# Optimization experiments

Measured on AMD Instinct MI355X. Metric: run time of the kernel, lower is better.

The kernel has to match this reference:

```python
import jax, jax.numpy as jnp
import numpy as np

D_MODEL = 768
D_STATE = 16
D_CONV = 4
EXPAND = 2
INNER = EXPAND * D_MODEL  # 1536
BATCH = 2
SEQLEN = 2048


def setup_inputs() -> dict:
    key = jax.random.key(0)
    ks = jax.random.split(key, 8)
    s = 0.02
    return {
        "hidden_states": jax.random.normal(ks[0], (BATCH, SEQLEN, D_MODEL), jnp.float32),
        "in_proj_w": jax.random.normal(ks[1], (2 * INNER, D_MODEL), jnp.float32) * (D_MODEL ** -0.5),
        "out_proj_w": jax.random.normal(ks[2], (D_MODEL, INNER), jnp.float32) * (INNER ** -0.5),
        "dt_proj_w": jax.random.normal(ks[3], (INNER, INNER), jnp.float32) * (INNER ** -0.5),
        "dt_proj_b": jnp.zeros((INNER,), jnp.float32),
        "conv_w": jax.random.normal(ks[4], (INNER, D_CONV), jnp.float32) * s,
        "conv_b": jnp.zeros((INNER,), jnp.float32),
        "A_log": jnp.zeros((INNER, D_STATE), jnp.float32),
        "B_param": jax.random.normal(ks[5], (INNER, D_STATE), jnp.float32) * s,
        "C_param": jax.random.normal(ks[6], (INNER, D_STATE), jnp.float32) * s,
        "D_param": jnp.ones((INNER,), jnp.float32),
        "dt_bias": jnp.zeros((INNER,), jnp.float32),
    }


def reference(hidden_states, in_proj_w, out_proj_w, dt_proj_w, dt_proj_b,
              conv_w, conv_b, A_log, B_param, C_param, D_param, dt_bias):
    # in_proj: (B, L, d_model) -> (B, L, 2*inner); split into projected / gate
    xz = jnp.einsum('bld,od->blo', hidden_states, in_proj_w)
    proj, gate = jnp.split(xz, 2, axis=-1)
    x = jnp.transpose(proj, (0, 2, 1))  # (B, inner, L) channel-first

    # depthwise causal conv (left-pad d_conv-1) + bias + SiLU
    conv = jax.lax.conv_general_dilated(
        x, conv_w[:, None, :], window_strides=(1,),
        padding=[(D_CONV - 1, 0)], feature_group_count=INNER,
        dimension_numbers=('NCH', 'OIH', 'NCH'))
    u = jax.nn.silu(conv + conv_b[None, :, None])  # (B, inner, L)

    # dt projection (1x1 linear on channel-first) + softplus(dt + dt_bias)
    delta = jnp.einsum('oc,bcl->bol', dt_proj_w, u) + dt_proj_b[None, :, None]
    dt = jax.nn.softplus(delta + dt_bias[None, :, None])  # (B, inner, L)

    A = -jnp.exp(A_log)  # (inner, d_state)
    # discretize: dA = exp(dt * A), dBu = dt * u * B   -> (B, inner, L, N)
    dA = jnp.exp(dt[..., None] * A[None, :, None, :])
    dBu = (dt * u)[..., None] * B_param[None, :, None, :]

    dA_t = jnp.moveaxis(dA, 2, 0)    # (L, B, inner, N)
    dBu_t = jnp.moveaxis(dBu, 2, 0)  # (L, B, inner, N)

    def step(h, inp):
        a_t, b_t = inp
        h = a_t * h + b_t                      # (B, inner, N)
        y = jnp.einsum('bdn,dn->bd', h, C_param)
        return h, y

    h0 = jnp.zeros(dA_t.shape[1:], dA.dtype)
    _, ys = jax.lax.scan(step, h0, (dA_t, dBu_t))  # ys: (L, B, inner)
    y = jnp.transpose(ys, (1, 2, 0))               # (B, inner, L)

    z = jnp.transpose(gate, (0, 2, 1))             # (B, inner, L)
    y = (y + D_param[None, :, None] * u) * jax.nn.silu(z)

    # out_proj: (B, inner, L) -> (B, L, d_model)
    return jnp.einsum('bdl,od->blo', y, out_proj_w)
```

## Files before the change

kernel.cpp:

```cpp
#include <hip/hip_runtime.h>
#include <cstdint>
#include <cstddef>

#define D_MODEL 768
#define D_STATE 16
#define D_CONV  4
#define INNER   1536
#define BATCH   2
#define SEQLEN  2048
#define M_TOK   (BATCH * SEQLEN)
#define NCH     (BATCH * INNER)
#define NCHUNK  64
#define CL      (SEQLEN / NCHUNK)

typedef unsigned short u16;
typedef __attribute__((ext_vector_type(4))) unsigned short us4;
typedef __attribute__((ext_vector_type(8))) short bf8;
typedef __attribute__((ext_vector_type(4))) float f32x4;

__device__ __forceinline__ u16 f2bf(float f) {
    uint32_t x = __float_as_uint(f);
    return (u16)((x + 0x7fffu + ((x >> 16) & 1u)) >> 16);
}
__device__ __forceinline__ float bf2f(u16 h) {
    return __uint_as_float(((uint32_t)h) << 16);
}

__global__ __launch_bounds__(256) void cvt_hilo4(
    const float* __restrict__ s0, u16* __restrict__ h0, u16* __restrict__ l0, int n0,
    const float* __restrict__ s1, u16* __restrict__ h1, u16* __restrict__ l1, int n1,
    const float* __restrict__ s2, u16* __restrict__ h2, u16* __restrict__ l2, int n2,
    const float* __restrict__ s3, u16* __restrict__ h3, u16* __restrict__ l3, int n3)
{
    int j = blockIdx.x * 256 + threadIdx.x;
    const float* s; u16* hh; u16* ll;
    if (j < n0) { s = s0; hh = h0; ll = l0; }
    else {
        j -= n0;
        if (j < n1) { s = s1; hh = h1; ll = l1; }
        else {
            j -= n1;
            if (j < n2) { s = s2; hh = h2; ll = l2; }
            else {
                j -= n2;
                if (j >= n3) return;
                s = s3; hh = h3; ll = l3;
            }
        }
    }
    const float4 v = ((const float4*)s)[j];
    us4 h, l;
    h.x = f2bf(v.x); l.x = f2bf(v.x - bf2f(h.x));
    h.y = f2bf(v.y); l.y = f2bf(v.y - bf2f(h.y));
    h.z = f2bf(v.z); l.z = f2bf(v.z - bf2f(h.z));
    h.w = f2bf(v.w); l.w = f2bf(v.w - bf2f(h.w));
    ((us4*)hh)[j] = h;
    ((us4*)ll)[j] = l;
}

template <int MODE, int FRM, int FRN>
__global__ __launch_bounds__(256) void gemm_mfma(
    const u16* __restrict__ Ah_g, const u16* __restrict__ Al_g,
    const u16* __restrict__ Bh_g, const u16* __restrict__ Bl_g,
    float* __restrict__ C, const float* __restrict__ bias1,
    const float* __restrict__ bias2, int M, int N, int K)
{
    constexpr int BM = FRM * 32;
    constexpr int BN = FRN * 32;
    constexpr int SBUF = (BM + BN) * 128;
    __shared__ __align__(16) char smem[2 * SBUF];

    const int tid = threadIdx.x;
    const int w = tid >> 6;
    const int lane = tid & 63;

    const int gx = gridDim.x;
    const int nwg = gx * gridDim.y;
    int f = blockIdx.y * gx + blockIdx.x;
    f = (f & 7) * (nwg >> 3) + (f >> 3);
    const int bm = (f / gx) * BM;
    const int bn = (f % gx) * BN;

    const int wm = (w >> 1) * (FRM * 16);
    const int wn = (w & 1) * (FRN * 16);

    const int g8 = lane & 7;
    const int r8 = lane >> 3;
    const int srcg = g8 ^ r8;
    const int scol = (srcg & 3) * 8;
    const bool use_lo = (srcg & 4) != 0;

    const u16* pA[FRM];
    const u16* pB[FRN];
#pragma unroll
    for (int c = 0; c < FRM; ++c) {
        const int row = w * (FRM * 8) + c * 8 + r8;
        pA[c] = (use_lo ? Al_g : Ah_g) + (size_t)(bm + row) * K + scol;
    }
#pragma unroll
    for (int c = 0; c < FRN; ++c) {
        const int row = w * (FRN * 8) + c * 8 + r8;
        pB[c] = (use_lo ? Bl_g : Bh_g) + (size_t)(bn + row) * K + scol;
    }

    f32x4 acc[FRM][FRN] = {};
    const int fr = lane & 15;
    const int gk = lane >> 4;
    const int ghi = gk ^ (fr & 7);

    const int aoff_h = (wm + fr) * 128 + ghi * 16;
    const int aoff_l = (wm + fr) * 128 + (ghi ^ 4) * 16;
    const int boff_h = BM * 128 + (wn + fr) * 128 + ghi * 16;
    const int boff_l = BM * 128 + (wn + fr) * 128 + (ghi ^ 4) * 16;
    const char* const S0 = smem;
    const char* const S1 = smem + SBUF;

    const int nt = K >> 5;

#define STAGE_ALL(sb, kt)                                                           \
    {                                                                               \
        _Pragma("unroll")                                                           \
        for (int c = 0; c < FRM; ++c)                                               \
            __builtin_amdgcn_global_load_lds(                                       \
                (const __attribute__((address_space(1))) void*)(pA[c] + (kt)),      \
                (__attribute__((address_space(3))) void*)((char*)(sb) + (w * FRM + c) * 1024), \
                16, 0, 0);                                                          \
        _Pragma("unroll")                                                           \
        for (int c = 0; c < FRN; ++c)                                               \
            __builtin_amdgcn_global_load_lds(                                       \
                (const __attribute__((address_space(1))) void*)(pB[c] + (kt)),      \
                (__attribute__((address_space(3))) void*)((char*)(sb) + BM * 128 + (w * FRN + c) * 1024), \
                16, 0, 0);                                                          \
    }

#define WAIT_COUNTED()                                                              \
    if constexpr (FRM + FRN == 8) { asm volatile("s_waitcnt vmcnt(8)" ::: "memory"); } \
    else if constexpr (FRM + FRN == 6) { asm volatile("s_waitcnt vmcnt(6)" ::: "memory"); } \
    else { asm volatile("s_waitcnt vmcnt(4)" ::: "memory"); }

#define COMPUTE(S)                                                                  \
    {                                                                               \
        bf8 ah[FRM], al[FRM], bh[FRN], bl[FRN];                                     \
        _Pragma("unroll")                                                           \
        for (int i = 0; i < FRM; ++i) {                                             \
            ah[i] = *(const bf8*)((S) + aoff_h + i * 2048);                         \
            al[i] = *(const bf8*)((S) + aoff_l + i * 2048);                         \
        }                                                                           \
        _Pragma("unroll")                                                           \
        for (int j = 0; j < FRN; ++j) {                                             \
            bh[j] = *(const bf8*)((S) + boff_h + j * 2048);                         \
            bl[j] = *(const bf8*)((S) + boff_l + j * 2048);                         \
        }                                                                           \
        _Pragma("unroll")                                                           \
        for (int i = 0; i < FRM; ++i)                                               \
            _Pragma("unroll")                                                       \
            for (int j = 0; j < FRN; ++j) {                                         \
                acc[i][j] = __builtin_amdgcn_mfma_f32_16x16x32_bf16(ah[i], bh[j], acc[i][j], 0, 0, 0); \
                acc[i][j] = __builtin_amdgcn_mfma_f32_16x16x32_bf16(ah[i], bl[j], acc[i][j], 0, 0, 0); \
                acc[i][j] = __builtin_amdgcn_mfma_f32_16x16x32_bf16(al[i], bh[j], acc[i][j], 0, 0, 0); \
            }                                                                       \
    }

    STAGE_ALL(S0, 0)

    for (int t = 0; t < nt; t += 2) {
        STAGE_ALL(S1, (t + 1) * 32)
        WAIT_COUNTED()
        __builtin_amdgcn_s_barrier();
        __builtin_amdgcn_sched_barrier(0);
        __builtin_amdgcn_s_setprio(1);
        COMPUTE(S0)
        __builtin_amdgcn_s_setprio(0);
        __builtin_amdgcn_sched_barrier(0);
        __builtin_amdgcn_s_barrier();

        const int k2 = (t + 2 < nt) ? (t + 2) * 32 : (nt - 1) * 32;
        STAGE_ALL(S0, k2)
        WAIT_COUNTED()
        __builtin_amdgcn_s_barrier();
        __builtin_amdgcn_sched_barrier(0);
        __builtin_amdgcn_s_setprio(1);
        COMPUTE(S1)
        __builtin_amdgcn_s_setprio(0);
        __builtin_amdgcn_sched_barrier(0);
        __builtin_amdgcn_s_barrier();
    }
#undef STAGE_ALL
#undef WAIT_COUNTED
#undef COMPUTE

    const int r0 = (lane >> 4) * 4;
#pragma unroll
    for (int i = 0; i < FRM; ++i) {
        const int row0 = bm + wm + i * 16 + r0;
#pragma unroll
        for (int j = 0; j < FRN; ++j) {
            const int col = bn + wn + j * 16 + fr;
            float add = 0.f;
            if constexpr (MODE == 1) add = bias1[col] + bias2[col];
#pragma unroll
            for (int r = 0; r < 4; ++r) {
                float v = acc[i][j][r];
                if constexpr (MODE == 1) {
                    const float xx = v + add;
                    v = (xx > 20.f) ? xx : log1pf(expf(xx));
                }
                C[(size_t)(row0 + r) * N + col] = v;
            }
        }
    }
}

__global__ __launch_bounds__(256) void conv_silu_kernel(
    const float* __restrict__ xz, const float* __restrict__ cw,
    const float* __restrict__ cb, u16* __restrict__ uh, u16* __restrict__ ul)
{
    const int idx = blockIdx.x * 256 + threadIdx.x;
    const int c4 = (idx % (INNER / 4)) * 4;
    const int m  = idx / (INNER / 4);
    if (m >= M_TOK) return;
    const int b = m >> 11;
    const int l = m & (SEQLEN - 1);

    float wt[4][4];
#pragma unroll
    for (int i = 0; i < 4; ++i) {
        const float4 wv = *(const float4*)&cw[(c4 + i) * 4];
        wt[i][0] = wv.x; wt[i][1] = wv.y; wt[i][2] = wv.z; wt[i][3] = wv.w;
    }
    const float4 bias = *(const float4*)&cb[c4];
    float a[4] = {bias.x, bias.y, bias.z, bias.w};

#pragma unroll
    for (int j = 0; j < 4; ++j) {
        const int ll = l - 3 + j;
        if (ll >= 0) {
            const float4 x = *(const float4*)&xz[(size_t)(b * SEQLEN + ll) * (2 * INNER) + c4];
            a[0] = fmaf(x.x, wt[0][j], a[0]);
            a[1] = fmaf(x.y, wt[1][j], a[1]);
            a[2] = fmaf(x.z, wt[2][j], a[2]);
            a[3] = fmaf(x.w, wt[3][j], a[3]);
        }
    }
    float o[4];
#pragma unroll
    for (int i = 0; i < 4; ++i) o[i] = a[i] / (1.f + __expf(-a[i]));

    us4 h, lo;
    h.x = f2bf(o[0]); lo.x = f2bf(o[0] - bf2f(h.x));
    h.y = f2bf(o[1]); lo.y = f2bf(o[1] - bf2f(h.y));
    h.z = f2bf(o[2]); lo.z = f2bf(o[2] - bf2f(h.z));
    h.w = f2bf(o[3]); lo.w = f2bf(o[3] - bf2f(h.w));
    const size_t vi = ((size_t)m * INNER + c4) / 4;
    ((us4*)uh)[vi] = h;
    ((us4*)ul)[vi] = lo;
}

__global__ __launch_bounds__(256) void scan_pass1(
    const float* __restrict__ dt, const u16* __restrict__ uh,
    const u16* __restrict__ ul, const float* __restrict__ A_log,
    const float* __restrict__ Bp, float* __restrict__ hend,
    float* __restrict__ Sdt)
{
    const int ch = blockIdx.x * 256 + threadIdx.x;
    const int c = blockIdx.y;
    const int b = (ch >= INNER) ? 1 : 0;
    const int d = ch - b * INNER;

    float A2[D_STATE], Bn[D_STATE];
#pragma unroll
    for (int n = 0; n < D_STATE; n += 4) {
        const float4 av = *(const float4*)&A_log[d * D_STATE + n];
        const float4 bv = *(const float4*)&Bp[d * D_STATE + n];
        A2[n+0] = -expf(av.x) * 1.44269504f; Bn[n+0] = bv.x;
        A2[n+1] = -expf(av.y) * 1.44269504f; Bn[n+1] = bv.y;
        A2[n+2] = -expf(av.z) * 1.44269504f; Bn[n+2] = bv.z;
        A2[n+3] = -expf(av.w) * 1.44269504f; Bn[n+3] = bv.w;
    }

    const size_t base = (size_t)(b * SEQLEN + c * CL) * INNER + d;
    const float* dtp = dt + base;
    const u16* uhp = uh + base;
    const u16* ulp = ul + base;

    float h[D_STATE] = {};
    float S = 0.f;

    float dtv = dtp[0];
    float uv = bf2f(uhp[0]) + bf2f(ulp[0]);

    for (int l = 0; l < CL; ++l) {
        float dtn = 0.f, un = 0.f;
        if (l + 1 < CL) {
            dtn = dtp[(size_t)(l + 1) * INNER];
            un = bf2f(uhp[(size_t)(l + 1) * INNER]) + bf2f(ulp[(size_t)(l + 1) * INNER]);
        }
        const float dtu = dtv * uv;
        S += dtv;
#pragma unroll
        for (int n = 0; n < D_STATE; ++n) {
            const float dA = exp2f(dtv * A2[n]);
            h[n] = fmaf(dA, h[n], dtu * Bn[n]);
        }
        dtv = dtn; uv = un;
    }

#pragma unroll
    for (int n = 0; n < D_STATE; ++n)
        hend[((size_t)c * D_STATE + n) * NCH + ch] = h[n];
    Sdt[(size_t)c * NCH + ch] = S;
}

__global__ __launch_bounds__(256) void scan_combine(
    const float* __restrict__ hend, const float* __restrict__ Sdt,
    const float* __restrict__ A_log, float* __restrict__ h0all)
{
    const int idx = blockIdx.x * 256 + threadIdx.x;
    const int n = idx / NCH;
    const int ch = idx - n * NCH;
    const int b = (ch >= INNER) ? 1 : 0;
    const int d = ch - b * INNER;
    const float A2 = -expf(A_log[d * D_STATE + n]) * 1.44269504f;

    float h0 = 0.f;
    for (int c = 0; c < NCHUNK; ++c) {
        const size_t o = ((size_t)c * D_STATE + n) * NCH + ch;
        h0all[o] = h0;
        const float P = exp2f(A2 * Sdt[(size_t)c * NCH + ch]);
        h0 = fmaf(P, h0, hend[o]);
    }
}

__global__ __launch_bounds__(256) void scan_pass2(
    const float* __restrict__ dt, const u16* __restrict__ uh,
    const u16* __restrict__ ul, const float* __restrict__ xz,
    const float* __restrict__ A_log, const float* __restrict__ Bp,
    const float* __restrict__ Cp, const float* __restrict__ Dp,
    const float* __restrict__ h0all, u16* __restrict__ ygh,
    u16* __restrict__ ygl)
{
    const int ch = blockIdx.x * 256 + threadIdx.x;
    const int c = blockIdx.y;
    const int b = (ch >= INNER) ? 1 : 0;
    const int d = ch - b * INNER;

    float A2[D_STATE], Bn[D_STATE], Cn[D_STATE];
#pragma unroll
    for (int n = 0; n < D_STATE; n += 4) {
        const float4 av = *(const float4*)&A_log[d * D_STATE + n];
        const float4 bv = *(const float4*)&Bp[d * D_STATE + n];
        const float4 cv = *(const float4*)&Cp[d * D_STATE + n];
        A2[n+0] = -expf(av.x) * 1.44269504f; Bn[n+0] = bv.x; Cn[n+0] = cv.x;
        A2[n+1] = -expf(av.y) * 1.44269504f; Bn[n+1] = bv.y; Cn[n+1] = cv.y;
        A2[n+2] = -expf(av.z) * 1.44269504f; Bn[n+2] = bv.z; Cn[n+2] = cv.z;
        A2[n+3] = -expf(av.w) * 1.44269504f; Bn[n+3] = bv.w; Cn[n+3] = cv.w;
    }
    const float Dd = Dp[d];

    float h[D_STATE];
#pragma unroll
    for (int n = 0; n < D_STATE; ++n)
        h[n] = h0all[((size_t)c * D_STATE + n) * NCH + ch];

    const size_t base = (size_t)(b * SEQLEN + c * CL) * INNER + d;
    const float* dtp = dt + base;
    const u16* uhp = uh + base;
    const u16* ulp = ul + base;
    const float* zp = xz + (size_t)(b * SEQLEN + c * CL) * (2 * INNER) + INNER + d;
    u16* yhp = ygh + base;
    u16* ylp = ygl + base;

    float dtv = dtp[0];
    float uv = bf2f(uhp[0]) + bf2f(ulp[0]);
    float zv = zp[0];

    for (int l = 0; l < CL; ++l) {
        float dtn = 0.f, un = 0.f, zn = 0.f;
        if (l + 1 < CL) {
            dtn = dtp[(size_t)(l + 1) * INNER];
            un = bf2f(uhp[(size_t)(l + 1) * INNER]) + bf2f(ulp[(size_t)(l + 1) * INNER]);
            zn = zp[(size_t)(l + 1) * (2 * INNER)];
        }
        const float dtu = dtv * uv;
        float y = 0.f;
#pragma unroll
        for (int n = 0; n < D_STATE; ++n) {
            const float dA = exp2f(dtv * A2[n]);
            h[n] = fmaf(dA, h[n], dtu * Bn[n]);
            y = fmaf(h[n], Cn[n], y);
        }
        const float sig = 1.f / (1.f + __expf(-zv));
        const float val = (y + Dd * uv) * (zv * sig);
        const u16 hv = f2bf(val);
        yhp[(size_t)l * INNER] = hv;
        ylp[(size_t)l * INNER] = f2bf(val - bf2f(hv));
        dtv = dtn; uv = un; zv = zn;
    }
}

extern "C" void kernel_launch(void* const* d_in, const int* in_sizes, int n_in,
                              void* d_out, int out_size, void* d_ws, size_t ws_size,
                              hipStream_t stream)
{
    const float* hs      = (const float*)d_in[0];
    const float* in_w    = (const float*)d_in[1];
    const float* out_w   = (const float*)d_in[2];
    const float* dt_w    = (const float*)d_in[3];
    const float* dt_b    = (const float*)d_in[4];
    const float* conv_w  = (const float*)d_in[5];
    const float* conv_b  = (const float*)d_in[6];
    const float* A_log   = (const float*)d_in[7];
    const float* Bp      = (const float*)d_in[8];
    const float* Cp      = (const float*)d_in[9];
    const float* Dp      = (const float*)d_in[10];
    const float* dt_bias = (const float*)d_in[11];
    float* out = (float*)d_out;

    float* xz    = (float*)d_ws;
    float* dtf   = xz + (size_t)M_TOK * 2 * INNER;
    float* hend  = dtf + (size_t)M_TOK * INNER;
    float* Sdt   = hend + (size_t)NCHUNK * D_STATE * NCH;
    float* h0all = Sdt + (size_t)NCHUNK * NCH;
    u16* uh  = (u16*)(h0all + (size_t)NCHUNK * D_STATE * NCH);
    u16* ul  = uh  + (size_t)M_TOK * INNER;
    u16* hsh = ul  + (size_t)M_TOK * INNER;
    u16* hsl = hsh + (size_t)M_TOK * D_MODEL;
    u16* ygh = hsl + (size_t)M_TOK * D_MODEL;
    u16* ygl = ygh + (size_t)M_TOK * INNER;
    u16* iwh = ygl + (size_t)M_TOK * INNER;
    u16* iwl = iwh + (size_t)2 * INNER * D_MODEL;
    u16* dwh = iwl + (size_t)2 * INNER * D_MODEL;
    u16* dwl = dwh + (size_t)INNER * INNER;
    u16* owh = dwl + (size_t)INNER * INNER;
    u16* owl = owh + (size_t)D_MODEL * INNER;

    const dim3 blk(256);

    {
        const int n0 = M_TOK * D_MODEL / 4;
        const int n1 = 2 * INNER * D_MODEL / 4;
        const int n2 = INNER * INNER / 4;
        const int n3 = D_MODEL * INNER / 4;
        const int ntot = n0 + n1 + n2 + n3;
        cvt_hilo4<<<dim3((ntot + 255) / 256), blk, 0, stream>>>(
            hs, hsh, hsl, n0, in_w, iwh, iwl, n1,
            dt_w, dwh, dwl, n2, out_w, owh, owl, n3);
    }

    gemm_mfma<0, 4, 4><<<dim3(2 * INNER / 128, M_TOK / 128), blk, 0, stream>>>(
        hsh, hsl, iwh, iwl, xz, nullptr, nullptr, M_TOK, 2 * INNER, D_MODEL);

    conv_silu_kernel<<<dim3((M_TOK * (INNER / 4)) / 256), blk, 0, stream>>>(
        xz, conv_w, conv_b, uh, ul);

    gemm_mfma<1, 4, 2><<<dim3(INNER / 64, M_TOK / 128), blk, 0, stream>>>(
        uh, ul, dwh, dwl, dtf, dt_b, dt_bias, M_TOK, INNER, INNER);

    scan_pass1<<<dim3(NCH / 256, NCHUNK), blk, 0, stream>>>(
        dtf, uh, ul, A_log, Bp, hend, Sdt);
    scan_combine<<<dim3((D_STATE * NCH) / 256), blk, 0, stream>>>(
        hend, Sdt, A_log, h0all);
    scan_pass2<<<dim3(NCH / 256, NCHUNK), blk, 0, stream>>>(
        dtf, uh, ul, xz, A_log, Bp, Cp, Dp, h0all, ygh, ygl);

    gemm_mfma<0, 2, 2><<<dim3(D_MODEL / 64, M_TOK / 64), blk, 0, stream>>>(
        ygh, ygl, owh, owl, out, nullptr, nullptr, M_TOK, D_MODEL, INNER);
}
```

Baseline: 331.8 us.

## Replace bf16 hi/lo split GEMMs with two-level int8 quantized MFMA GEMMs

The in_proj and dt_proj GEMMs switch from bf16 hi/lo split MFMA to per-row int8 two-level quantization (coarse plus residual scaled by 254), using i8 MFMA with three products per tile. The conv+SiLU kernel now quantizes each token row to int8 pairs with a per-row scale, and the scan kernels dequantize u from these. This halves the operand bytes and uses the faster int8 MFMA path, and conversion is split into per-matrix rowquant launches. The price is reduced precision (about 15 bits effective), extra reduction work for row maxima, and more launches.

```diff
diff --git a/kernel.cpp b/kernel.cpp
--- a/kernel.cpp
+++ b/kernel.cpp
@@ -17,6 +17,9 @@
 typedef __attribute__((ext_vector_type(4))) unsigned short us4;
 typedef __attribute__((ext_vector_type(8))) short bf8;
 typedef __attribute__((ext_vector_type(4))) float f32x4;
+typedef __attribute__((ext_vector_type(4))) int i32x4;
+
+#define INV254 (1.f / 254.f)
 
 __device__ __forceinline__ u16 f2bf(float f) {
     uint32_t x = __float_as_uint(f);
@@ -25,37 +28,224 @@
 __device__ __forceinline__ float bf2f(u16 h) {
     return __uint_as_float(((uint32_t)h) << 16);
 }
-
-__global__ __launch_bounds__(256) void cvt_hilo4(
-    const float* __restrict__ s0, u16* __restrict__ h0, u16* __restrict__ l0, int n0,
-    const float* __restrict__ s1, u16* __restrict__ h1, u16* __restrict__ l1, int n1,
-    const float* __restrict__ s2, u16* __restrict__ h2, u16* __restrict__ l2, int n2,
-    const float* __restrict__ s3, u16* __restrict__ h3, u16* __restrict__ l3, int n3)
-{
-    int j = blockIdx.x * 256 + threadIdx.x;
-    const float* s; u16* hh; u16* ll;
-    if (j < n0) { s = s0; hh = h0; ll = l0; }
-    else {
-        j -= n0;
-        if (j < n1) { s = s1; hh = h1; ll = l1; }
-        else {
-            j -= n1;
-            if (j < n2) { s = s2; hh = h2; ll = l2; }
-            else {
-                j -= n2;
-                if (j >= n3) return;
-                s = s3; hh = h3; ll = l3;
-            }
-        }
-    }
-    const float4 v = ((const float4*)s)[j];
+__device__ __forceinline__ int pk8(float a, float b, float c, float d) {
+    return ((int)a & 0xff) | (((int)b & 0xff) << 8) |
+           (((int)c & 0xff) << 16) | (((int)d & 0xff) << 24);
+}
+
+__global__ __launch_bounds__(256) void rowquant(
+    const float* __restrict__ src, int8_t* __restrict__ q1,
+    int8_t* __restrict__ q0, float* __restrict__ sc, int K)
+{
+    const int row = blockIdx.x;
+    const float* r = src + (size_t)row * K;
+    const int tid = threadIdx.x;
+
+    float mx = 0.f;
+    for (int i = tid * 4; i < K; i += 1024) {
+        const float4 v = *(const float4*)(r + i);
+        mx = fmaxf(mx, fmaxf(fmaxf(fabsf(v.x), fabsf(v.y)),
+                             fmaxf(fabsf(v.z), fabsf(v.w))));
+    }
+#pragma unroll
+    for (int off = 1; off < 64; off <<= 1)
+        mx = fmaxf(mx, __shfl_xor(mx, off, 64));
+    __shared__ float red[4];
+    if ((tid & 63) == 0) red[tid >> 6] = mx;
+    __syncthreads();
+    const float rm = fmaxf(fmaxf(red[0], red[1]), fmaxf(red[2], red[3]));
+    const float q = rm > 0.f ? 127.f / rm : 0.f;
+
+    for (int i = tid * 4; i < K; i += 1024) {
+        const float4 v = *(const float4*)(r + i);
+        float s1[4], s0[4];
+        const float xv[4] = {v.x, v.y, v.z, v.w};
+#pragma unroll
+        for (int e = 0; e < 4; ++e) {
+            const float t = xv[e] * q;
+            s1[e] = rintf(t);
+            s0[e] = rintf((t - s1[e]) * 254.f);
+        }
+        const size_t o = ((size_t)row * K + i) >> 2;
+        ((int*)q1)[o] = pk8(s1[0], s1[1], s1[2], s1[3]);
+        ((int*)q0)[o] = pk8(s0[0], s0[1], s0[2], s0[3]);
+    }
+    if (tid == 0) sc[row] = rm * (1.f / 127.f);
+}
+
+__global__ __launch_bounds__(256) void cvt_hilo(
+    const float* __restrict__ x, u16* __restrict__ hi, u16* __restrict__ lo, int n4)
+{
+    const int i = blockIdx.x * 256 + threadIdx.x;
+    if (i >= n4) return;
+    const float4 v = ((const float4*)x)[i];
     us4 h, l;
     h.x = f2bf(v.x); l.x = f2bf(v.x - bf2f(h.x));
     h.y = f2bf(v.y); l.y = f2bf(v.y - bf2f(h.y));
     h.z = f2bf(v.z); l.z = f2bf(v.z - bf2f(h.z));
     h.w = f2bf(v.w); l.w = f2bf(v.w - bf2f(h.w));
-    ((us4*)hh)[j] = h;
-    ((us4*)ll)[j] = l;
+    ((us4*)hi)[i] = h;
+    ((us4*)lo)[i] = l;
+}
+
+template <int MODE, int FRM, int FRN>
+__global__ __launch_bounds__(256) void gemm_i8(
+    const int8_t* __restrict__ A1g, const int8_t* __restrict__ A0g,
+    const int8_t* __restrict__ B1g, const int8_t* __restrict__ B0g,
+    const float* __restrict__ scA, const float* __restrict__ scB,
+    float* __restrict__ C, const float* __restrict__ bias1,
+    const float* __restrict__ bias2, int M, int N, int K)
+{
+    constexpr int BM = FRM * 32;
+    constexpr int BN = FRN * 32;
+    constexpr int SBUF = (BM + BN) * 128;
+    __shared__ __align__(16) char smem[2 * SBUF];
+
+    const int tid = threadIdx.x;
+    const int w = tid >> 6;
+    const int lane = tid & 63;
+
+    const int gx = gridDim.x;
+    const int nwg = gx * gridDim.y;
+    int f = blockIdx.y * gx + blockIdx.x;
+    f = (f & 7) * (nwg >> 3) + (f >> 3);
+    const int bm = (f / gx) * BM;
+    const int bn = (f % gx) * BN;
+
+    const int wm = (w >> 1) * (FRM * 16);
+    const int wn = (w & 1) * (FRN * 16);
+
+    const int g8 = lane & 7;
+    const int r8 = lane >> 3;
+    const int srcg = g8 ^ r8;
+    const int sbyte = (srcg & 3) * 16;
+    const bool use_lo = (srcg & 4) != 0;
+
+    const int8_t* pA[FRM];
+    const int8_t* pB[FRN];
+#pragma unroll
+    for (int c = 0; c < FRM; ++c) {
+        const int row = w * (FRM * 8) + c * 8 + r8;
+        pA[c] = (use_lo ? A0g : A1g) + (size_t)(bm + row) * K + sbyte;
+    }
+#pragma unroll
+    for (int c = 0; c < FRN; ++c) {
+        const int row = w * (FRN * 8) + c * 8 + r8;
+        pB[c] = (use_lo ? B0g : B1g) + (size_t)(bn + row) * K + sbyte;
+    }
+
+    i32x4 acc1[FRM][FRN] = {};
+    i32x4 acc2[FRM][FRN] = {};
+    const int fr = lane & 15;
+    const int gk = lane >> 4;
+    const int ghi = gk ^ (fr & 7);
+
+    const int aoff1 = (wm + fr) * 128 + ghi * 16;
+    const int aoff0 = (wm + fr) * 128 + (ghi ^ 4) * 16;
+    const int boff1 = BM * 128 + (wn + fr) * 128 + ghi * 16;
+    const int boff0 = BM * 128 + (wn + fr) * 128 + (ghi ^ 4) * 16;
+    const char* const S0 = smem;
+    const char* const S1 = smem + SBUF;
+
+    const int nt = K >> 6;
+
+#define STAGE_ALL(sb, kt)                                                           \
+    {                                                                               \
+        _Pragma("unroll")                                                           \
+        for (int c = 0; c < FRM; ++c)                                               \
+            __builtin_amdgcn_global_load_lds(                                       \
+                (const __attribute__((address_space(1))) void*)(pA[c] + (kt)),      \
+                (__attribute__((address_space(3))) void*)((char*)(sb) + (w * FRM + c) * 1024), \
+                16, 0, 0);                                                          \
+        _Pragma("unroll")                                                           \
+        for (int c = 0; c < FRN; ++c)                                               \
+            __builtin_amdgcn_global_load_lds(                                       \
+                (const __attribute__((address_space(1))) void*)(pB[c] + (kt)),      \
+                (__attribute__((address_space(3))) void*)((char*)(sb) + BM * 128 + (w * FRN + c) * 1024), \
+                16, 0, 0);                                                          \
+    }
+
+#define WAIT_COUNTED()                                                              \
+    if constexpr (FRM + FRN == 8) { asm volatile("s_waitcnt vmcnt(8)" ::: "memory"); } \
+    else if constexpr (FRM + FRN == 6) { asm volatile("s_waitcnt vmcnt(6)" ::: "memory"); } \
+    else { asm volatile("s_waitcnt vmcnt(4)" ::: "memory"); }
+
+#define COMPUTE(S)                                                                  \
+    {                                                                               \
+        i32x4 a1[FRM], a0[FRM], b1[FRN], b0[FRN];                                   \
+        _Pragma("unroll")                                                           \
+        for (int i = 0; i < FRM; ++i) {                                             \
+            a1[i] = *(const i32x4*)((S) + aoff1 + i * 2048);                        \
+            a0[i] = *(const i32x4*)((S) + aoff0 + i * 2048);                        \
+        }                                                                           \
+        _Pragma("unroll")                                                           \
+        for (int j = 0; j < FRN; ++j) {                                             \
+            b1[j] = *(const i32x4*)((S) + boff1 + j * 2048);                        \
+            b0[j] = *(const i32x4*)((S) + boff0 + j * 2048);                        \
+        }                                                                           \
+        _Pragma("unroll")                                                           \
+        for (int i = 0; i < FRM; ++i)                                               \
+            _Pragma("unroll")                                                       \
+            for (int j = 0; j < FRN; ++j) {                                         \
+                acc1[i][j] = __builtin_amdgcn_mfma_i32_16x16x64_i8(a1[i], b1[j], acc1[i][j], 0, 0, 0); \
+                acc2[i][j] = __builtin_amdgcn_mfma_i32_16x16x64_i8(a1[i], b0[j], acc2[i][j], 0, 0, 0); \
+                acc2[i][j] = __builtin_amdgcn_mfma_i32_16x16x64_i8(a0[i], b1[j], acc2[i][j], 0, 0, 0); \
+            }                                                                       \
+    }
+
+    STAGE_ALL(S0, 0)
+
+    for (int t = 0; t < nt; t += 2) {
+        STAGE_ALL(S1, (t + 1) * 64)
+        WAIT_COUNTED()
+        __builtin_amdgcn_s_barrier();
+        __builtin_amdgcn_sched_barrier(0);
+        __builtin_amdgcn_s_setprio(1);
+        COMPUTE(S0)
+        __builtin_amdgcn_s_setprio(0);
+        __builtin_amdgcn_sched_barrier(0);
+        __builtin_amdgcn_s_barrier();
+
+        const int k2 = (t + 2 < nt) ? (t + 2) * 64 : (nt - 1) * 64;
+        STAGE_ALL(S0, k2)
+        WAIT_COUNTED()
+        __builtin_amdgcn_s_barrier();
+        __builtin_amdgcn_sched_barrier(0);
+        __builtin_amdgcn_s_setprio(1);
+        COMPUTE(S1)
+        __builtin_amdgcn_s_setprio(0);
+        __builtin_amdgcn_sched_barrier(0);
+        __builtin_amdgcn_s_barrier();
+    }
+#undef STAGE_ALL
+#undef WAIT_COUNTED
+#undef COMPUTE
+
+    const int r0 = (lane >> 4) * 4;
+#pragma unroll
+    for (int i = 0; i < FRM; ++i) {
+        const int row0 = bm + wm + i * 16 + r0;
+        float sA[4];
+#pragma unroll
+        for (int r = 0; r < 4; ++r) sA[r] = scA[row0 + r];
+#pragma unroll
+        for (int j = 0; j < FRN; ++j) {
+            const int col = bn + wn + j * 16 + fr;
+            const float sB = scB[col];
+            float add = 0.f;
+            if constexpr (MODE == 1) add = bias1[col] + bias2[col];
+#pragma unroll
+            for (int r = 0; r < 4; ++r) {
+                float v = ((float)acc1[i][j][r] +
+                           (float)acc2[i][j][r] * INV254) * (sA[r] * sB);
+                if constexpr (MODE == 1) {
+                    const float xx = v + add;
+                    v = (xx > 20.f) ? xx : log1pf(expf(xx));
+                }
+                C[(size_t)(row0 + r) * N + col] = v;
+            }
+        }
+    }
 }
 
 template <int MODE, int FRM, int FRN>
@@ -211,14 +401,14 @@
     }
 }
 
-__global__ __launch_bounds__(256) void conv_silu_kernel(
+__global__ __launch_bounds__(384) void conv_silu_quant(
     const float* __restrict__ xz, const float* __restrict__ cw,
-    const float* __restrict__ cb, u16* __restrict__ uh, u16* __restrict__ ul)
-{
-    const int idx = blockIdx.x * 256 + threadIdx.x;
-    const int c4 = (idx % (INNER / 4)) * 4;
-    const int m  = idx / (INNER / 4);
-    if (m >= M_TOK) return;
+    const float* __restrict__ cb, int8_t* __restrict__ u1,
+    int8_t* __restrict__ u0, float* __restrict__ su)
+{
+    const int m = blockIdx.x;
+    const int tid = threadIdx.x;
+    const int c4 = tid * 4;
     const int b = m >> 11;
     const int l = m & (SEQLEN - 1);
 
@@ -246,21 +436,37 @@
 #pragma unroll
     for (int i = 0; i < 4; ++i) o[i] = a[i] / (1.f + __expf(-a[i]));
 
-    us4 h, lo;
-    h.x = f2bf(o[0]); lo.x = f2bf(o[0] - bf2f(h.x));
-    h.y = f2bf(o[1]); lo.y = f2bf(o[1] - bf2f(h.y));
-    h.z = f2bf(o[2]); lo.z = f2bf(o[2] - bf2f(h.z));
-    h.w = f2bf(o[3]); lo.w = f2bf(o[3] - bf2f(h.w));
-    const size_t vi = ((size_t)m * INNER + c4) / 4;
-    ((us4*)uh)[vi] = h;
-    ((us4*)ul)[vi] = lo;
+    float mx = fmaxf(fmaxf(fabsf(o[0]), fabsf(o[1])),
+                     fmaxf(fabsf(o[2]), fabsf(o[3])));
+#pragma unroll
+    for (int off = 1; off < 64; off <<= 1)
+        mx = fmaxf(mx, __shfl_xor(mx, off, 64));
+    __shared__ float red[6];
+    if ((tid & 63) == 0) red[tid >> 6] = mx;
+    __syncthreads();
+    float rm = red[0];
+#pragma unroll
+    for (int i = 1; i < 6; ++i) rm = fmaxf(rm, red[i]);
+    const float q = rm > 0.f ? 127.f / rm : 0.f;
+
+    float s1[4], s0[4];
+#pragma unroll
+    for (int e = 0; e < 4; ++e) {
+        const float t = o[e] * q;
+        s1[e] = rintf(t);
+        s0[e] = rintf((t - s1[e]) * 254.f);
+    }
+    const size_t vi = ((size_t)m * INNER + c4) >> 2;
+    ((int*)u1)[vi] = pk8(s1[0], s1[1], s1[2], s1[3]);
+    ((int*)u0)[vi] = pk8(s0[0], s0[1], s0[2], s0[3]);
+    if (tid == 0) su[m] = rm * (1.f / 127.f);
 }
 
 __global__ __launch_bounds__(256) void scan_pass1(
-    const float* __restrict__ dt, const u16* __restrict__ uh,
-    const u16* __restrict__ ul, const float* __restrict__ A_log,
-    const float* __restrict__ Bp, float* __restrict__ hend,
-    float* __restrict__ Sdt)
+    const float* __restrict__ dt, const int8_t* __restrict__ u1,
+    const int8_t* __restrict__ u0, const float* __restrict__ su,
+    const float* __restrict__ A_log, const float* __restrict__ Bp,
+    float* __restrict__ hend, float* __restrict__ Sdt)
 {
     const int ch = blockIdx.x * 256 + threadIdx.x;
     const int c = blockIdx.y;
@@ -280,20 +486,22 @@
 
     const size_t base = (size_t)(b * SEQLEN + c * CL) * INNER + d;
     const float* dtp = dt + base;
-    const u16* uhp = uh + base;
-    const u16* ulp = ul + base;
+    const int8_t* u1p = u1 + base;
+    const int8_t* u0p = u0 + base;
+    const float* sup = su + (b * SEQLEN + c * CL);
 
     float h[D_STATE] = {};
     float S = 0.f;
 
     float dtv = dtp[0];
-    float uv = bf2f(uhp[0]) + bf2f(ulp[0]);
+    float uv = fmaf((float)u0p[0], INV254, (float)u1p[0]) * sup[0];
 
     for (int l = 0; l < CL; ++l) {
         float dtn = 0.f, un = 0.f;
         if (l + 1 < CL) {
             dtn = dtp[(size_t)(l + 1) * INNER];
-            un = bf2f(uhp[(size_t)(l + 1) * INNER]) + bf2f(ulp[(size_t)(l + 1) * INNER]);
+            un = fmaf((float)u0p[(size_t)(l + 1) * INNER], INV254,
+                      (float)u1p[(size_t)(l + 1) * INNER]) * sup[l + 1];
         }
         const float dtu = dtv * uv;
         S += dtv;
@@ -332,12 +540,12 @@
 }
 
 __global__ __launch_bounds__(256) void scan_pass2(
-    const float* __restrict__ dt, const u16* __restrict__ uh,
-    const u16* __restrict__ ul, const float* __restrict__ xz,
-    const float* __restrict__ A_log, const float* __restrict__ Bp,
-    const float* __restrict__ Cp, const float* __restrict__ Dp,
-    const float* __restrict__ h0all, u16* __restrict__ ygh,
-    u16* __restrict__ ygl)
+    const float* __restrict__ dt, const int8_t* __restrict__ u1,
+    const int8_t* __restrict__ u0, const float* __restrict__ su,
+    const float* __restrict__ xz, const float* __restrict__ A_log,
+    const float* __restrict__ Bp, const float* __restrict__ Cp,
+    const float* __restrict__ Dp, const float* __restrict__ h0all,
+    u16* __restrict__ ygh, u16* __restrict__ ygl)
 {
     const int ch = blockIdx.x * 256 + threadIdx.x;
     const int c = blockIdx.y;
@@ -364,21 +572,23 @@
 
     const size_t base = (size_t)(b * SEQLEN + c * CL) * INNER + d;
     const float* dtp = dt + base;
-    const u16* uhp = uh + base;
-    const u16* ulp = ul + base;
+    const int8_t* u1p = u1 + base;
+    const int8_t* u0p = u0 + base;
+    const float* sup = su + (b * SEQLEN + c * CL);
     const float* zp = xz + (size_t)(b * SEQLEN + c * CL) * (2 * INNER) + INNER + d;
     u16* yhp = ygh + base;
     u16* ylp = ygl + base;
 
     float dtv = dtp[0];
-    float uv = bf2f(uhp[0]) + bf2f(ulp[0]);
+    float uv = fmaf((float)u0p[0], INV254, (float)u1p[0]) * sup[0];
     float zv = zp[0];
 
     for (int l = 0; l < CL; ++l) {
         float dtn = 0.f, un = 0.f, zn = 0.f;
         if (l + 1 < CL) {
             dtn = dtp[(size_t)(l + 1) * INNER];
-            un = bf2f(uhp[(size_t)(l + 1) * INNER]) + bf2f(ulp[(size_t)(l + 1) * INNER]);
+            un = fmaf((float)u0p[(size_t)(l + 1) * INNER], INV254,
+                      (float)u1p[(size_t)(l + 1) * INNER]) * sup[l + 1];
             zn = zp[(size_t)(l + 1) * (2 * INNER)];
         }
         const float dtu = dtv * uv;
@@ -421,47 +631,48 @@
     float* hend  = dtf + (size_t)M_TOK * INNER;
     float* Sdt   = hend + (size_t)NCHUNK * D_STATE * NCH;
     float* h0all = Sdt + (size_t)NCHUNK * NCH;
-    u16* uh  = (u16*)(h0all + (size_t)NCHUNK * D_STATE * NCH);
-    u16* ul  = uh  + (size_t)M_TOK * INNER;
-    u16* hsh = ul  + (size_t)M_TOK * INNER;
-    u16* hsl = hsh + (size_t)M_TOK * D_MODEL;
-    u16* ygh = hsl + (size_t)M_TOK * D_MODEL;
+    float* su_u  = h0all + (size_t)NCHUNK * D_STATE * NCH;
+    float* sc_hs = su_u + M_TOK;
+    float* sc_iw = sc_hs + M_TOK;
+    float* sc_dw = sc_iw + 2 * INNER;
+    u16* ygh = (u16*)(sc_dw + INNER);
     u16* ygl = ygh + (size_t)M_TOK * INNER;
-    u16* iwh = ygl + (size_t)M_TOK * INNER;
-    u16* iwl = iwh + (size_t)2 * INNER * D_MODEL;
-    u16* dwh = iwl + (size_t)2 * INNER * D_MODEL;
-    u16* dwl = dwh + (size_t)INNER * INNER;
-    u16* owh = dwl + (size_t)INNER * INNER;
+    u16* owh = ygl + (size_t)M_TOK * INNER;
     u16* owl = owh + (size_t)D_MODEL * INNER;
+    int8_t* hs1 = (int8_t*)(owl + (size_t)D_MODEL * INNER);
+    int8_t* hs0 = hs1 + (size_t)M_TOK * D_MODEL;
+    int8_t* iw1 = hs0 + (size_t)M_TOK * D_MODEL;
+    int8_t* iw0 = iw1 + (size_t)2 * INNER * D_MODEL;
+    int8_t* dw1 = iw0 + (size_t)2 * INNER * D_MODEL;
+    int8_t* dw0 = dw1 + (size_t)INNER * INNER;
+    int8_t* u1  = dw0 + (size_t)INNER * INNER;
+    int8_t* u0  = u1 + (size_t)M_TOK * INNER;
 
     const dim3 blk(256);
 
-    {
-        const int n0 = M_TOK * D_MODEL / 4;
-        const int n1 = 2 * INNER * D_MODEL / 4;
-        const int n2 = INNER * INNER / 4;
-        const int n3 = D_MODEL * INNER / 4;
-        const int ntot = n0 + n1 + n2 + n3;
-        cvt_hilo4<<<dim3((ntot + 255) / 256), blk, 0, stream>>>(
-            hs, hsh, hsl, n0, in_w, iwh, iwl, n1,
-            dt_w, dwh, dwl, n2, out_w, owh, owl, n3);
-    }
-
-    gemm_mfma<0, 4, 4><<<dim3(2 * INNER / 128, M_TOK / 128), blk, 0, stream>>>(
-        hsh, hsl, iwh, iwl, xz, nullptr, nullptr, M_TOK, 2 * INNER, D_MODEL);
-
-    conv_silu_kernel<<<dim3((M_TOK * (INNER / 4)) / 256), blk, 0, stream>>>(
-        xz, conv_w, conv_b, uh, ul);
-
-    gemm_mfma<1, 4, 2><<<dim3(INNER / 64, M_TOK / 128), blk, 0, stream>>>(
-        uh, ul, dwh, dwl, dtf, dt_b, dt_bias, M_TOK, INNER, INNER);
+    rowquant<<<dim3(M_TOK), blk, 0, stream>>>(hs, hs1, hs0, sc_hs, D_MODEL);
+    rowquant<<<dim3(2 * INNER), blk, 0, stream>>>(in_w, iw1, iw0, sc_iw, D_MODEL);
+    rowquant<<<dim3(INNER), blk, 0, stream>>>(dt_w, dw1, dw0, sc_dw, INNER);
+    cvt_hilo<<<dim3((D_MODEL * INNER / 4 + 255) / 256), blk, 0, stream>>>(
+        out_w, owh, owl, D_MODEL * INNER / 4);
+
+    gemm_i8<0, 4, 4><<<dim3(2 * INNER / 128, M_TOK / 128), blk, 0, stream>>>(
+        hs1, hs0, iw1, iw0, sc_hs, sc_iw, xz, nullptr, nullptr,
+        M_TOK, 2 * INNER, D_MODEL);
+
+    conv_silu_quant<<<dim3(M_TOK), dim3(384), 0, stream>>>(
+        xz, conv_w, conv_b, u1, u0, su_u);
+
+    gemm_i8<1, 4, 2><<<dim3(INNER / 64, M_TOK / 128), blk, 0, stream>>>(
+        u1, u0, dw1, dw0, su_u, sc_dw, dtf, dt_b, dt_bias,
+        M_TOK, INNER, INNER);
 
     scan_pass1<<<dim3(NCH / 256, NCHUNK), blk, 0, stream>>>(
-        dtf, uh, ul, A_log, Bp, hend, Sdt);
+        dtf, u1, u0, su_u, A_log, Bp, hend, Sdt);
     scan_combine<<<dim3((D_STATE * NCH) / 256), blk, 0, stream>>>(
         hend, Sdt, A_log, h0all);
     scan_pass2<<<dim3(NCH / 256, NCHUNK), blk, 0, stream>>>(
-        dtf, uh, ul, xz, A_log, Bp, Cp, Dp, h0all, ygh, ygl);
+        dtf, u1, u0, su_u, xz, A_log, Bp, Cp, Dp, h0all, ygh, ygl);
 
     gemm_mfma<0, 2, 2><<<dim3(D_MODEL / 64, M_TOK / 64), blk, 0, stream>>>(
         ygh, ygl, owh, owl, out, nullptr, nullptr, M_TOK, D_MODEL, INNER);
```

Result: faster. 303.6 us (-8.5%).
